# Performance work log

Hardware: AMD Instinct MI355X
Metric: run time of the kernel (lower is better)

Reference implementation:

```python
import jax, jax.numpy as jnp
from jax import lax
import numpy as np

B = 262144      # batch (scaled from toy 10)
T = 5           # timesteps, hard-coded in source reshape [_, 5, 1]
D_IN = 1        # input feature dim
UNITS = 64      # LSTM units (scaled from toy 10)


def setup_inputs() -> dict:
    key = jax.random.key(0)
    ks = jax.random.split(key, 5)
    x = jax.random.normal(ks[0], (B, T, D_IN), dtype=jnp.float32)
    # Keras LSTM params: kernel [D_IN, 4*units], recurrent_kernel [units, 4*units], bias [4*units]
    W = jax.random.normal(ks[1], (D_IN, 4 * UNITS), dtype=jnp.float32) * 0.5
    U = jax.random.normal(ks[2], (UNITS, 4 * UNITS), dtype=jnp.float32) * (1.0 / np.sqrt(UNITS))
    b = jnp.zeros((4 * UNITS,), dtype=jnp.float32)
    Wd = jax.random.normal(ks[3], (UNITS, 1), dtype=jnp.float32) * (1.0 / np.sqrt(UNITS))
    bd = jnp.zeros((1,), dtype=jnp.float32)
    return {"x": x, "W": W, "U": U, "b": b, "Wd": Wd, "bd": bd}


def reference(x, W, U, b, Wd, bd):
    # Faithful to: x = reshape(input, [B, T, 1]); x = LSTM(units)(x); out = Dense(1, relu)(x)
    units = U.shape[0]
    batch = x.shape[0]
    xs = jnp.transpose(x, (1, 0, 2))  # [T, B, D_IN] for scan over time

    def step(carry, xt):
        h, c = carry
        z = xt @ W + h @ U + b            # [B, 4*units]
        i, f, g, o = jnp.split(z, 4, axis=-1)  # Keras gate order: i, f, c~, o
        i = jax.nn.sigmoid(i)
        f = jax.nn.sigmoid(f)
        g = jnp.tanh(g)
        o = jax.nn.sigmoid(o)
        c = f * c + i * g
        h = o * jnp.tanh(c)
        return (h, c), None

    h0 = jnp.zeros((batch, units), dtype=x.dtype)
    (h_last, _), _ = lax.scan(step, (h0, h0), xs)
    # Dense(1, activation='relu')
    return jax.nn.relu(h_last @ Wd + bd)  # [B, 1]
```

## Files before the change

kernel.cpp:

```cpp
#include <hip/hip_runtime.h>


typedef _Float16 f16x8 __attribute__((ext_vector_type(8)));
typedef float f32x4 __attribute__((ext_vector_type(4)));
typedef float f32x2 __attribute__((ext_vector_type(2)));

#define MB 128
#define NTHREADS 256
#define HSTR 68

__device__ __forceinline__ float ex2(float x) { return __builtin_amdgcn_exp2f(x); }
__device__ __forceinline__ float rcp(float x) { return __builtin_amdgcn_rcpf(x); }
__device__ __forceinline__ f32x2 fma2(f32x2 a, f32x2 b, f32x2 c) {
    return __builtin_elementwise_fma(a, b, c);
}

__global__ __launch_bounds__(NTHREADS, 3) void lstm_fused(
    const float* __restrict__ x,
    const float* __restrict__ W,
    const float* __restrict__ U,
    const float* __restrict__ b,
    const float* __restrict__ Wd,
    const float* __restrict__ bd,
    float* __restrict__ out,
    int B)
{
    __shared__ _Float16 hbuf[2][2][64 * HSTR];
    __shared__ float xs[5][MB];
    __shared__ float red[2][MB];
    __shared__ float wds[64];

    const int tid  = threadIdx.x;
    const int wv   = tid >> 6;
    const int lane = tid & 63;
    const int l15  = lane & 15;
    const int quad = lane >> 4;
    const int row0 = blockIdx.x * MB;

    for (int i = tid; i < MB * 5; i += NTHREADS)
        xs[i % 5][i / 5] = x[row0 * 5 + i];
    if (tid < 64) wds[tid] = Wd[tid];

    const float LOG2E = 1.44269504f;
    const float gscale[4] = {-LOG2E, -LOG2E, -2.0f * LOG2E, -LOG2E};
    const float CSC = -2.0f * LOG2E;

    const int ncol = wv * 16 + l15;
    float Wf[4], bf[4];
    f16x8 Bf[4][2];
#pragma unroll
    for (int g = 0; g < 4; ++g) {
        const int n = g * 64 + ncol;
        const float s = gscale[g];
        Wf[g] = W[n] * s;
        bf[g] = b[n] * s;
#pragma unroll
        for (int kh = 0; kh < 2; ++kh) {
            f16x8 v;
#pragma unroll
            for (int j = 0; j < 8; ++j) {
                const int k = kh * 32 + quad * 8 + j;
                v[j] = (_Float16)(U[k * 256 + n] * s);
            }
            Bf[g][kh] = v;
            asm volatile("" : "+v"(Bf[g][kh]));
        }
    }

    f32x2 cst[2][4][2];
#pragma unroll
    for (int gr = 0; gr < 2; ++gr)
#pragma unroll
        for (int a = 0; a < 4; ++a)
#pragma unroll
            for (int pr = 0; pr < 2; ++pr) cst[gr][a][pr] = (f32x2){0.f, 0.f};

    __syncthreads();

#pragma unroll
    for (int gr = 0; gr < 2; ++gr) {
#pragma unroll
        for (int rt = 0; rt < 4; ++rt) {
            const f32x4 xv = *(const f32x4*)&xs[0][gr * 64 + rt * 16 + quad * 4];
#pragma unroll
            for (int pr = 0; pr < 2; ++pr) {
                const f32x2 xp = {xv[2 * pr], xv[2 * pr + 1]};
                const f32x2 zi = fma2(xp, (f32x2){Wf[0], Wf[0]}, (f32x2){bf[0], bf[0]});
                const f32x2 zg = fma2(xp, (f32x2){Wf[2], Wf[2]}, (f32x2){bf[2], bf[2]});
                const f32x2 zo = fma2(xp, (f32x2){Wf[3], Wf[3]}, (f32x2){bf[3], bf[3]});
                const f32x2 ei = {ex2(zi.x), ex2(zi.y)};
                const f32x2 eg = {ex2(zg.x), ex2(zg.y)};
                const f32x2 eo = {ex2(zo.x), ex2(zo.y)};
                const f32x2 pq = (1.0f + ei) * (1.0f + eg);
                const f32x2 r1 = {rcp(pq.x), rcp(pq.y)};
                const f32x2 cn = (1.0f - eg) * r1;
                cst[gr][rt][pr] = cn;
                const f32x2 sc = cn * CSC;
                const f32x2 ec = {ex2(sc.x), ex2(sc.y)};
                const f32x2 dn = (1.0f + eo) * (1.0f + ec);
                const f32x2 r2 = {rcp(dn.x), rcp(dn.y)};
                const f32x2 h2 = (1.0f - ec) * r2;
                const int rb = rt * 16 + quad * 4 + 2 * pr;
                hbuf[gr][0][rb * HSTR + ncol]       = (_Float16)h2.x;
                hbuf[gr][0][(rb + 1) * HSTR + ncol] = (_Float16)h2.y;
            }
        }
    }

#pragma unroll
    for (int t = 1; t < 5; ++t) {
        const int src = (t + 1) & 1;
        const int dst = t & 1;
        __syncthreads();
#pragma unroll
        for (int gr = 0; gr < 2; ++gr) {
#pragma unroll
            for (int rt = 0; rt < 4; ++rt) {
                const int arow = rt * 16 + l15;
                const f16x8 a0 = *(const f16x8*)&hbuf[gr][src][arow * HSTR + quad * 8];
                const f16x8 a1 = *(const f16x8*)&hbuf[gr][src][arow * HSTR + 32 + quad * 8];
                const f32x4 xv = *(const f32x4*)&xs[t][gr * 64 + rt * 16 + quad * 4];
                const f32x2 xlo = {xv[0], xv[1]};
                const f32x2 xhi = {xv[2], xv[3]};
                f32x4 acc[4];
#pragma unroll
                for (int g = 0; g < 4; ++g) {
                    const f32x2 wg = {Wf[g], Wf[g]};
                    const f32x2 bg = {bf[g], bf[g]};
                    const f32x2 zlo = fma2(xlo, wg, bg);
                    const f32x2 zhi = fma2(xhi, wg, bg);
                    f32x4 z = {zlo.x, zlo.y, zhi.x, zhi.y};
                    z = __builtin_amdgcn_mfma_f32_16x16x32_f16(a0, Bf[g][0], z, 0, 0, 0);
                    z = __builtin_amdgcn_mfma_f32_16x16x32_f16(a1, Bf[g][1], z, 0, 0, 0);
                    acc[g] = z;
                }
#pragma unroll
                for (int pr = 0; pr < 2; ++pr) {
                    const f32x2 ei = {ex2(acc[0][2 * pr]), ex2(acc[0][2 * pr + 1])};
                    const f32x2 ef = {ex2(acc[1][2 * pr]), ex2(acc[1][2 * pr + 1])};
                    const f32x2 eg = {ex2(acc[2][2 * pr]), ex2(acc[2][2 * pr + 1])};
                    const f32x2 eo = {ex2(acc[3][2 * pr]), ex2(acc[3][2 * pr + 1])};
                    const f32x2 p  = (1.0f + ei) * (1.0f + eg);
                    const f32x2 q  = 1.0f + ef;
                    const f32x2 num = fma2(cst[gr][rt][pr], p, q * (1.0f - eg));
                    const f32x2 pq  = p * q;
                    const f32x2 ipq = {rcp(pq.x), rcp(pq.y)};
                    const f32x2 cn  = num * ipq;
                    cst[gr][rt][pr] = cn;
                    const f32x2 sc = cn * CSC;
                    const f32x2 ec = {ex2(sc.x), ex2(sc.y)};
                    const f32x2 dn = (1.0f + eo) * (1.0f + ec);
                    const f32x2 r2 = {rcp(dn.x), rcp(dn.y)};
                    const f32x2 h2 = (1.0f - ec) * r2;
                    const int rb = rt * 16 + quad * 4 + 2 * pr;
                    hbuf[gr][dst][rb * HSTR + ncol]       = (_Float16)h2.x;
                    hbuf[gr][dst][(rb + 1) * HSTR + ncol] = (_Float16)h2.y;
                }
            }
        }
    }

    __syncthreads();

    {
        const int row = tid & 127;
        const int qh  = tid >> 7;
        const int gr  = row >> 6;
        const int rl  = row & 63;
        float s = 0.0f;
#pragma unroll
        for (int j = 0; j < 32; ++j)
            s += (float)hbuf[gr][0][rl * HSTR + qh * 32 + j] * wds[qh * 32 + j];
        red[qh][row] = s;
    }
    __syncthreads();
    if (tid < MB) {
        const float r = red[0][tid] + red[1][tid] + bd[0];
        out[row0 + tid] = fmaxf(r, 0.0f);
    }
}

extern "C" void kernel_launch(void* const* d_in, const int* in_sizes, int n_in,
                              void* d_out, int out_size, void* d_ws, size_t ws_size,
                              hipStream_t stream) {
    const float* x  = (const float*)d_in[0];
    const float* W  = (const float*)d_in[1];
    const float* U  = (const float*)d_in[2];
    const float* b  = (const float*)d_in[3];
    const float* Wd = (const float*)d_in[4];
    const float* bd = (const float*)d_in[5];
    float* out = (float*)d_out;
    const int B = in_sizes[0] / 5;
    const int grid = B / MB;
    lstm_fused<<<grid, NTHREADS, 0, stream>>>(x, W, U, b, Wd, bd, out, B);
}
```

Measured before the change: 142.1 us.

## Batch reciprocals across four pairs and prescale factors to share one rcp

Reworks the gate math so that four packed pairs from two row tiles share a single reciprocal. The product of their denominators is inverted once and each individual reciprocal is recovered by multiplying with the other factors. Factors are prescaled by 2^-30 and 2^-9 to keep the four-way products in range, and the (1+e) terms are rewritten as fmas. This is meant to cut transcendental rcp throughput pressure, at the cost of extra multiplies, more register pressure and some risk of overflow or underflow for extreme exp values.

```diff
diff --git a/kernel.cpp b/kernel.cpp
--- a/kernel.cpp
+++ b/kernel.cpp
@@ -13,6 +13,9 @@
 __device__ __forceinline__ float rcp(float x) { return __builtin_amdgcn_rcpf(x); }
 __device__ __forceinline__ f32x2 fma2(f32x2 a, f32x2 b, f32x2 c) {
     return __builtin_elementwise_fma(a, b, c);
+}
+__device__ __forceinline__ f32x2 ex22(f32x2 a) {
+    return (f32x2){ex2(a.x), ex2(a.y)};
 }
 
 __global__ __launch_bounds__(NTHREADS, 3) void lstm_fused(
@@ -44,6 +47,11 @@
     const float LOG2E = 1.44269504f;
     const float gscale[4] = {-LOG2E, -LOG2E, -2.0f * LOG2E, -LOG2E};
     const float CSC = -2.0f * LOG2E;
+    const f32x2 K30  = {0x1p-30f, 0x1p-30f};
+    const f32x2 C30  = {CSC * 0x1p-30f, CSC * 0x1p-30f};
+    const f32x2 NC30 = {-CSC * 0x1p-30f, -CSC * 0x1p-30f};
+    const f32x2 K9   = {0x1p-9f, 0x1p-9f};
+    const f32x2 NK9  = {-0x1p-9f, -0x1p-9f};
 
     const int ncol = wv * 16 + l15;
     float Wf[4], bf[4];
@@ -80,30 +88,69 @@
 #pragma unroll
     for (int gr = 0; gr < 2; ++gr) {
 #pragma unroll
-        for (int rt = 0; rt < 4; ++rt) {
-            const f32x4 xv = *(const f32x4*)&xs[0][gr * 64 + rt * 16 + quad * 4];
-#pragma unroll
-            for (int pr = 0; pr < 2; ++pr) {
-                const f32x2 xp = {xv[2 * pr], xv[2 * pr + 1]};
-                const f32x2 zi = fma2(xp, (f32x2){Wf[0], Wf[0]}, (f32x2){bf[0], bf[0]});
-                const f32x2 zg = fma2(xp, (f32x2){Wf[2], Wf[2]}, (f32x2){bf[2], bf[2]});
-                const f32x2 zo = fma2(xp, (f32x2){Wf[3], Wf[3]}, (f32x2){bf[3], bf[3]});
-                const f32x2 ei = {ex2(zi.x), ex2(zi.y)};
-                const f32x2 eg = {ex2(zg.x), ex2(zg.y)};
-                const f32x2 eo = {ex2(zo.x), ex2(zo.y)};
-                const f32x2 pq = (1.0f + ei) * (1.0f + eg);
-                const f32x2 r1 = {rcp(pq.x), rcp(pq.y)};
-                const f32x2 cn = (1.0f - eg) * r1;
-                cst[gr][rt][pr] = cn;
-                const f32x2 sc = cn * CSC;
-                const f32x2 ec = {ex2(sc.x), ex2(sc.y)};
-                const f32x2 dn = (1.0f + eo) * (1.0f + ec);
-                const f32x2 r2 = {rcp(dn.x), rcp(dn.y)};
-                const f32x2 h2 = (1.0f - ec) * r2;
-                const int rb = rt * 16 + quad * 4 + 2 * pr;
-                hbuf[gr][0][rb * HSTR + ncol]       = (_Float16)h2.x;
-                hbuf[gr][0][(rb + 1) * HSTR + ncol] = (_Float16)h2.y;
-            }
+        for (int rtp = 0; rtp < 2; ++rtp) {
+            const int rtA = 2 * rtp, rtB = 2 * rtp + 1;
+            const f32x4 xvA = *(const f32x4*)&xs[0][gr * 64 + rtA * 16 + quad * 4];
+            const f32x4 xvB = *(const f32x4*)&xs[0][gr * 64 + rtB * 16 + quad * 4];
+            const f32x2 wi = {Wf[0], Wf[0]}, bi = {bf[0], bf[0]};
+            const f32x2 wg = {Wf[2], Wf[2]}, bg = {bf[2], bf[2]};
+            const f32x2 wo = {Wf[3], Wf[3]}, bo = {bf[3], bf[3]};
+            const f32x2 xA0 = {xvA[0], xvA[1]}, xA1 = {xvA[2], xvA[3]};
+            const f32x2 xB0 = {xvB[0], xvB[1]}, xB1 = {xvB[2], xvB[3]};
+            const f32x2 eiA0 = ex22(fma2(xA0, wi, bi));
+            const f32x2 eiA1 = ex22(fma2(xA1, wi, bi));
+            const f32x2 eiB0 = ex22(fma2(xB0, wi, bi));
+            const f32x2 eiB1 = ex22(fma2(xB1, wi, bi));
+            const f32x2 egA0 = ex22(fma2(xA0, wg, bg));
+            const f32x2 egA1 = ex22(fma2(xA1, wg, bg));
+            const f32x2 egB0 = ex22(fma2(xB0, wg, bg));
+            const f32x2 egB1 = ex22(fma2(xB1, wg, bg));
+            const f32x2 eoA0 = ex22(fma2(xA0, wo, bo));
+            const f32x2 eoA1 = ex22(fma2(xA1, wo, bo));
+            const f32x2 eoB0 = ex22(fma2(xB0, wo, bo));
+            const f32x2 eoB1 = ex22(fma2(xB1, wo, bo));
+            const f32x2 PA0 = fma2(eiA0, K30, K30), PA1 = fma2(eiA1, K30, K30);
+            const f32x2 PB0 = fma2(eiB0, K30, K30), PB1 = fma2(eiB1, K30, K30);
+            const f32x2 pA0 = fma2(egA0, PA0, PA0), pA1 = fma2(egA1, PA1, PA1);
+            const f32x2 pB0 = fma2(egB0, PB0, PB0), pB1 = fma2(egB1, PB1, PB1);
+            const f32x2 wsA0 = fma2(egA0, NC30, C30), wsA1 = fma2(egA1, NC30, C30);
+            const f32x2 wsB0 = fma2(egB0, NC30, C30), wsB1 = fma2(egB1, NC30, C30);
+            const f32x2 mA = pA0 * pA1, mB = pB0 * pB1;
+            const f32x2 M  = mA * mB;
+            const f32x2 r  = {rcp(M.x), rcp(M.y)};
+            const f32x2 rA = r * mB, rB = r * mA;
+            const f32x2 csA0 = wsA0 * (rA * pA1);
+            const f32x2 csA1 = wsA1 * (rA * pA0);
+            const f32x2 csB0 = wsB0 * (rB * pB1);
+            const f32x2 csB1 = wsB1 * (rB * pB0);
+            cst[gr][rtA][0] = csA0; cst[gr][rtA][1] = csA1;
+            cst[gr][rtB][0] = csB0; cst[gr][rtB][1] = csB1;
+            const f32x2 ecA0 = ex22(csA0), ecA1 = ex22(csA1);
+            const f32x2 ecB0 = ex22(csB0), ecB1 = ex22(csB1);
+            const f32x2 AoA0 = fma2(eoA0, K9, K9), AoA1 = fma2(eoA1, K9, K9);
+            const f32x2 AoB0 = fma2(eoB0, K9, K9), AoB1 = fma2(eoB1, K9, K9);
+            const f32x2 dnA0 = fma2(ecA0, AoA0, AoA0), dnA1 = fma2(ecA1, AoA1, AoA1);
+            const f32x2 dnB0 = fma2(ecB0, AoB0, AoB0), dnB1 = fma2(ecB1, AoB1, AoB1);
+            const f32x2 omA0 = fma2(ecA0, NK9, K9), omA1 = fma2(ecA1, NK9, K9);
+            const f32x2 omB0 = fma2(ecB0, NK9, K9), omB1 = fma2(ecB1, NK9, K9);
+            const f32x2 m2A = dnA0 * dnA1, m2B = dnB0 * dnB1;
+            const f32x2 M2  = m2A * m2B;
+            const f32x2 r2  = {rcp(M2.x), rcp(M2.y)};
+            const f32x2 r2A = r2 * m2B, r2B = r2 * m2A;
+            const f32x2 hA0 = omA0 * (r2A * dnA1);
+            const f32x2 hA1 = omA1 * (r2A * dnA0);
+            const f32x2 hB0 = omB0 * (r2B * dnB1);
+            const f32x2 hB1 = omB1 * (r2B * dnB0);
+            const int rbA = rtA * 16 + quad * 4;
+            const int rbB = rtB * 16 + quad * 4;
+            hbuf[gr][0][(rbA + 0) * HSTR + ncol] = (_Float16)hA0.x;
+            hbuf[gr][0][(rbA + 1) * HSTR + ncol] = (_Float16)hA0.y;
+            hbuf[gr][0][(rbA + 2) * HSTR + ncol] = (_Float16)hA1.x;
+            hbuf[gr][0][(rbA + 3) * HSTR + ncol] = (_Float16)hA1.y;
+            hbuf[gr][0][(rbB + 0) * HSTR + ncol] = (_Float16)hB0.x;
+            hbuf[gr][0][(rbB + 1) * HSTR + ncol] = (_Float16)hB0.y;
+            hbuf[gr][0][(rbB + 2) * HSTR + ncol] = (_Float16)hB1.x;
+            hbuf[gr][0][(rbB + 3) * HSTR + ncol] = (_Float16)hB1.y;
         }
     }
 
@@ -115,47 +162,102 @@
 #pragma unroll
         for (int gr = 0; gr < 2; ++gr) {
 #pragma unroll
-            for (int rt = 0; rt < 4; ++rt) {
-                const int arow = rt * 16 + l15;
-                const f16x8 a0 = *(const f16x8*)&hbuf[gr][src][arow * HSTR + quad * 8];
-                const f16x8 a1 = *(const f16x8*)&hbuf[gr][src][arow * HSTR + 32 + quad * 8];
-                const f32x4 xv = *(const f32x4*)&xs[t][gr * 64 + rt * 16 + quad * 4];
-                const f32x2 xlo = {xv[0], xv[1]};
-                const f32x2 xhi = {xv[2], xv[3]};
-                f32x4 acc[4];
+            for (int rtp = 0; rtp < 2; ++rtp) {
+                const int rtA = 2 * rtp, rtB = 2 * rtp + 1;
+                const int arowA = rtA * 16 + l15;
+                const int arowB = rtB * 16 + l15;
+                const f16x8 a0A = *(const f16x8*)&hbuf[gr][src][arowA * HSTR + quad * 8];
+                const f16x8 a1A = *(const f16x8*)&hbuf[gr][src][arowA * HSTR + 32 + quad * 8];
+                const f16x8 a0B = *(const f16x8*)&hbuf[gr][src][arowB * HSTR + quad * 8];
+                const f16x8 a1B = *(const f16x8*)&hbuf[gr][src][arowB * HSTR + 32 + quad * 8];
+                const f32x4 xvA = *(const f32x4*)&xs[t][gr * 64 + rtA * 16 + quad * 4];
+                const f32x4 xvB = *(const f32x4*)&xs[t][gr * 64 + rtB * 16 + quad * 4];
+                const f32x2 xloA = {xvA[0], xvA[1]}, xhiA = {xvA[2], xvA[3]};
+                const f32x2 xloB = {xvB[0], xvB[1]}, xhiB = {xvB[2], xvB[3]};
+                f32x4 accA[4], accB[4];
 #pragma unroll
                 for (int g = 0; g < 4; ++g) {
-                    const f32x2 wg = {Wf[g], Wf[g]};
-                    const f32x2 bg = {bf[g], bf[g]};
-                    const f32x2 zlo = fma2(xlo, wg, bg);
-                    const f32x2 zhi = fma2(xhi, wg, bg);
-                    f32x4 z = {zlo.x, zlo.y, zhi.x, zhi.y};
-                    z = __builtin_amdgcn_mfma_f32_16x16x32_f16(a0, Bf[g][0], z, 0, 0, 0);
-                    z = __builtin_amdgcn_mfma_f32_16x16x32_f16(a1, Bf[g][1], z, 0, 0, 0);
-                    acc[g] = z;
+                    const f32x2 wgv = {Wf[g], Wf[g]};
+                    const f32x2 bgv = {bf[g], bf[g]};
+                    const f32x2 zloA = fma2(xloA, wgv, bgv);
+                    const f32x2 zhiA = fma2(xhiA, wgv, bgv);
+                    f32x4 zA = {zloA.x, zloA.y, zhiA.x, zhiA.y};
+                    zA = __builtin_amdgcn_mfma_f32_16x16x32_f16(a0A, Bf[g][0], zA, 0, 0, 0);
+                    zA = __builtin_amdgcn_mfma_f32_16x16x32_f16(a1A, Bf[g][1], zA, 0, 0, 0);
+                    accA[g] = zA;
+                    const f32x2 zloB = fma2(xloB, wgv, bgv);
+                    const f32x2 zhiB = fma2(xhiB, wgv, bgv);
+                    f32x4 zB = {zloB.x, zloB.y, zhiB.x, zhiB.y};
+                    zB = __builtin_amdgcn_mfma_f32_16x16x32_f16(a0B, Bf[g][0], zB, 0, 0, 0);
+                    zB = __builtin_amdgcn_mfma_f32_16x16x32_f16(a1B, Bf[g][1], zB, 0, 0, 0);
+                    accB[g] = zB;
                 }
-#pragma unroll
-                for (int pr = 0; pr < 2; ++pr) {
-                    const f32x2 ei = {ex2(acc[0][2 * pr]), ex2(acc[0][2 * pr + 1])};
-                    const f32x2 ef = {ex2(acc[1][2 * pr]), ex2(acc[1][2 * pr + 1])};
-                    const f32x2 eg = {ex2(acc[2][2 * pr]), ex2(acc[2][2 * pr + 1])};
-                    const f32x2 eo = {ex2(acc[3][2 * pr]), ex2(acc[3][2 * pr + 1])};
-                    const f32x2 p  = (1.0f + ei) * (1.0f + eg);
-                    const f32x2 q  = 1.0f + ef;
-                    const f32x2 num = fma2(cst[gr][rt][pr], p, q * (1.0f - eg));
-                    const f32x2 pq  = p * q;
-                    const f32x2 ipq = {rcp(pq.x), rcp(pq.y)};
-                    const f32x2 cn  = num * ipq;
-                    cst[gr][rt][pr] = cn;
-                    const f32x2 sc = cn * CSC;
-                    const f32x2 ec = {ex2(sc.x), ex2(sc.y)};
-                    const f32x2 dn = (1.0f + eo) * (1.0f + ec);
-                    const f32x2 r2 = {rcp(dn.x), rcp(dn.y)};
-                    const f32x2 h2 = (1.0f - ec) * r2;
-                    const int rb = rt * 16 + quad * 4 + 2 * pr;
-                    hbuf[gr][dst][rb * HSTR + ncol]       = (_Float16)h2.x;
-                    hbuf[gr][dst][(rb + 1) * HSTR + ncol] = (_Float16)h2.y;
-                }
+                const f32x2 eiA0 = {ex2(accA[0][0]), ex2(accA[0][1])};
+                const f32x2 eiA1 = {ex2(accA[0][2]), ex2(accA[0][3])};
+                const f32x2 efA0 = {ex2(accA[1][0]), ex2(accA[1][1])};
+                const f32x2 efA1 = {ex2(accA[1][2]), ex2(accA[1][3])};
+                const f32x2 egA0 = {ex2(accA[2][0]), ex2(accA[2][1])};
+                const f32x2 egA1 = {ex2(accA[2][2]), ex2(accA[2][3])};
+                const f32x2 eoA0 = {ex2(accA[3][0]), ex2(accA[3][1])};
+                const f32x2 eoA1 = {ex2(accA[3][2]), ex2(accA[3][3])};
+                const f32x2 eiB0 = {ex2(accB[0][0]), ex2(accB[0][1])};
+                const f32x2 eiB1 = {ex2(accB[0][2]), ex2(accB[0][3])};
+                const f32x2 efB0 = {ex2(accB[1][0]), ex2(accB[1][1])};
+                const f32x2 efB1 = {ex2(accB[1][2]), ex2(accB[1][3])};
+                const f32x2 egB0 = {ex2(accB[2][0]), ex2(accB[2][1])};
+                const f32x2 egB1 = {ex2(accB[2][2]), ex2(accB[2][3])};
+                const f32x2 eoB0 = {ex2(accB[3][0]), ex2(accB[3][1])};
+                const f32x2 eoB1 = {ex2(accB[3][2]), ex2(accB[3][3])};
+                const f32x2 PA0 = fma2(eiA0, K30, K30), PA1 = fma2(eiA1, K30, K30);
+                const f32x2 PB0 = fma2(eiB0, K30, K30), PB1 = fma2(eiB1, K30, K30);
+                const f32x2 pA0 = fma2(egA0, PA0, PA0), pA1 = fma2(egA1, PA1, PA1);
+                const f32x2 pB0 = fma2(egB0, PB0, PB0), pB1 = fma2(egB1, PB1, PB1);
+                const f32x2 wsA0 = fma2(egA0, NC30, C30), wsA1 = fma2(egA1, NC30, C30);
+                const f32x2 wsB0 = fma2(egB0, NC30, C30), wsB1 = fma2(egB1, NC30, C30);
+                const f32x2 qwA0 = fma2(efA0, wsA0, wsA0), qwA1 = fma2(efA1, wsA1, wsA1);
+                const f32x2 qwB0 = fma2(efB0, wsB0, wsB0), qwB1 = fma2(efB1, wsB1, wsB1);
+                const f32x2 pqA0 = fma2(efA0, pA0, pA0), pqA1 = fma2(efA1, pA1, pA1);
+                const f32x2 pqB0 = fma2(efB0, pB0, pB0), pqB1 = fma2(efB1, pB1, pB1);
+                const f32x2 numsA0 = fma2(cst[gr][rtA][0], pA0, qwA0);
+                const f32x2 numsA1 = fma2(cst[gr][rtA][1], pA1, qwA1);
+                const f32x2 numsB0 = fma2(cst[gr][rtB][0], pB0, qwB0);
+                const f32x2 numsB1 = fma2(cst[gr][rtB][1], pB1, qwB1);
+                const f32x2 mA = pqA0 * pqA1, mB = pqB0 * pqB1;
+                const f32x2 M  = mA * mB;
+                const f32x2 r  = {rcp(M.x), rcp(M.y)};
+                const f32x2 rA = r * mB, rB = r * mA;
+                const f32x2 csA0 = numsA0 * (rA * pqA1);
+                const f32x2 csA1 = numsA1 * (rA * pqA0);
+                const f32x2 csB0 = numsB0 * (rB * pqB1);
+                const f32x2 csB1 = numsB1 * (rB * pqB0);
+                cst[gr][rtA][0] = csA0; cst[gr][rtA][1] = csA1;
+                cst[gr][rtB][0] = csB0; cst[gr][rtB][1] = csB1;
+                const f32x2 ecA0 = ex22(csA0), ecA1 = ex22(csA1);
+                const f32x2 ecB0 = ex22(csB0), ecB1 = ex22(csB1);
+                const f32x2 AoA0 = fma2(eoA0, K9, K9), AoA1 = fma2(eoA1, K9, K9);
+                const f32x2 AoB0 = fma2(eoB0, K9, K9), AoB1 = fma2(eoB1, K9, K9);
+                const f32x2 dnA0 = fma2(ecA0, AoA0, AoA0), dnA1 = fma2(ecA1, AoA1, AoA1);
+                const f32x2 dnB0 = fma2(ecB0, AoB0, AoB0), dnB1 = fma2(ecB1, AoB1, AoB1);
+                const f32x2 omA0 = fma2(ecA0, NK9, K9), omA1 = fma2(ecA1, NK9, K9);
+                const f32x2 omB0 = fma2(ecB0, NK9, K9), omB1 = fma2(ecB1, NK9, K9);
+                const f32x2 m2A = dnA0 * dnA1, m2B = dnB0 * dnB1;
+                const f32x2 M2  = m2A * m2B;
+                const f32x2 r2  = {rcp(M2.x), rcp(M2.y)};
+                const f32x2 r2A = r2 * m2B, r2B = r2 * m2A;
+                const f32x2 hA0 = omA0 * (r2A * dnA1);
+                const f32x2 hA1 = omA1 * (r2A * dnA0);
+                const f32x2 hB0 = omB0 * (r2B * dnB1);
+                const f32x2 hB1 = omB1 * (r2B * dnB0);
+                const int rbA = rtA * 16 + quad * 4;
+                const int rbB = rtB * 16 + quad * 4;
+                hbuf[gr][dst][(rbA + 0) * HSTR + ncol] = (_Float16)hA0.x;
+                hbuf[gr][dst][(rbA + 1) * HSTR + ncol] = (_Float16)hA0.y;
+                hbuf[gr][dst][(rbA + 2) * HSTR + ncol] = (_Float16)hA1.x;
+                hbuf[gr][dst][(rbA + 3) * HSTR + ncol] = (_Float16)hA1.y;
+                hbuf[gr][dst][(rbB + 0) * HSTR + ncol] = (_Float16)hB0.x;
+                hbuf[gr][dst][(rbB + 1) * HSTR + ncol] = (_Float16)hB0.y;
+                hbuf[gr][dst][(rbB + 2) * HSTR + ncol] = (_Float16)hB1.x;
+                hbuf[gr][dst][(rbB + 3) * HSTR + ncol] = (_Float16)hB1.y;
             }
         }
     }
```

New measurement: 137.1 us. -3.5%, faster.
